# Kernel tuning notes

Measured on AMD Instinct MI355X. Metric: run time of the kernel, lower is better.

Reference implementation:

```python
import jax, jax.numpy as jnp
import numpy as np

N_NODES = 20000
N_EDGES = 320000
N_GRAPHS = 64
IN_FEAT = 64
HIDDEN = 256
GRID = 4
NUM_LAYERS = 4  # -> 3 Fourier message-passing layers
NEG_SLOPE = 0.01  # nn.LeakyReLU default


def setup_inputs() -> dict:
    key = jax.random.key(0)
    ks = jax.random.split(key, 8)
    h = jax.random.normal(ks[0], (N_NODES, IN_FEAT), dtype=jnp.float32)
    src = jax.random.randint(ks[1], (N_EDGES,), 0, N_NODES, dtype=jnp.int32)
    dst = jax.random.randint(ks[2], (N_EDGES,), 0, N_NODES, dtype=jnp.int32)
    graph_ids = jnp.sort(jax.random.randint(ks[3], (N_NODES,), 0, N_GRAPHS, dtype=jnp.int32))
    # KAN_polynomial(in_feat, hidden, degree=grid_feat), init randn/(sqrt(in)*sqrt(deg))
    W_line = jax.random.normal(ks[4], (HIDDEN, IN_FEAT, GRID + 1), dtype=jnp.float32) / (
        np.sqrt(IN_FEAT) * np.sqrt(GRID))
    # 3 NaiveFourierKANLayer coeffs [2, out, in, grid]
    fourier_coeffs = jax.random.normal(ks[5], (NUM_LAYERS - 1, 2, HIDDEN, HIDDEN, GRID),
                                       dtype=jnp.float32) / (np.sqrt(HIDDEN) * np.sqrt(GRID))
    # Readout KAN_polynomial(hidden, 1, degree=1, addbias=True)
    W_out = jax.random.normal(ks[6], (1, HIDDEN, 2), dtype=jnp.float32) / np.sqrt(HIDDEN)
    b_out = jnp.zeros((1, 1), dtype=jnp.float32)
    return {"h": h, "src": src, "dst": dst, "graph_ids": graph_ids,
            "W_line": W_line, "fourier_coeffs": fourier_coeffs,
            "W_out": W_out, "b_out": b_out}


def kan_polynomial(x, coeffs, bias=None):
    # x: [b, in], coeffs: [out, in, deg+1]
    deg = coeffs.shape[-1] - 1
    powers = jnp.stack([x ** i for i in range(deg + 1)], axis=-1)  # [b, in, deg+1]
    y = jnp.einsum('bid,oid->bo', powers, coeffs)
    if bias is not None:
        y = y + bias
    return y


def fourier_kan(x, coeffs):
    # x: [N, in], coeffs: [2, out, in, grid]
    grid = coeffs.shape[-1]
    k = jnp.arange(1, grid + 1, dtype=x.dtype)  # [grid]
    ang = x[:, :, None] * k  # [N, in, grid]
    y = jnp.einsum('nig,oig->no', jnp.cos(ang), coeffs[0])
    y = y + jnp.einsum('nig,oig->no', jnp.sin(ang), coeffs[1])
    return y


def reference(h, src, dst, graph_ids, W_line, fourier_coeffs, W_out, b_out):
    # kan_line
    h = kan_polynomial(h, W_line)  # [N, hidden]
    # message-passing Fourier KAN layers with residual + leaky_relu
    for l in range(NUM_LAYERS - 1):
        agg = jax.ops.segment_sum(h[src], dst, num_segments=N_NODES)  # copy_u + sum
        m = fourier_kan(agg, fourier_coeffs[l])
        h = jax.nn.leaky_relu(m + h, negative_slope=NEG_SLOPE)
    # avg pooling per graph
    sums = jax.ops.segment_sum(h, graph_ids, num_segments=N_GRAPHS)  # [G, hidden]
    counts = jax.ops.segment_sum(jnp.ones((N_NODES,), dtype=h.dtype), graph_ids,
                                 num_segments=N_GRAPHS)
    y = sums / jnp.maximum(counts, 1.0)[:, None]
    # Readout: KAN_polynomial(hidden, 1, degree=1) + sigmoid
    out = jax.nn.sigmoid(kan_polynomial(y, W_out, b_out))  # [G, 1]
    return out
```

## Files before the change

### kernel.cpp

```cpp
#include <hip/hip_runtime.h>
#include <math.h>

#define N_NODES   20000
#define N_PAD2    20096
#define N_EDGES   320000
#define N_GRAPHS  64
#define IN_FEAT   64
#define HIDDEN    256
#define GRID_F    4
#define NLAYERS   3
#define NEG_SLOPE 0.01f

#define KF 2048
#define KL4 256
#define NB_SCAN 79
#define NRG  157
#define NBLK (NRG * 4)
#define NLBLK 1256

typedef _Float16 f16x8 __attribute__((ext_vector_type(8)));
typedef _Float16 f16x2 __attribute__((ext_vector_type(2)));
typedef float    f32x4 __attribute__((ext_vector_type(4)));

__global__ void transpose_fourier_f16(const float* __restrict__ fc, _Float16* __restrict__ Bt) {
    int idx = blockIdx.x * 256 + threadIdx.x;
    int kk  = idx & 2047;
    int rest = idx >> 11;
    int o = rest & 255;
    int l = rest >> 8;
    int i = kk >> 3, f = kk & 7, g = f >> 1, t = f & 1;
    Bt[idx] = (_Float16)fc[(((size_t)(l * 2 + t) * HIDDEN + o) * HIDDEN + i) * GRID_F + g];
}

__global__ void transpose_line4(const float* __restrict__ wl, _Float16* __restrict__ Wth,
                                _Float16* __restrict__ Wtl) {
    int idx = blockIdx.x * 256 + threadIdx.x;
    int o = idx >> 8, kk = idx & 255;
    int i = kk >> 2, d = (kk & 3) + 1;
    float wv = wl[(o * IN_FEAT + i) * 5 + d];
    _Float16 h = (_Float16)wv;
    Wth[idx] = h;
    Wtl[idx] = (_Float16)(wv - (float)h);
}

__global__ void line_bias(const float* __restrict__ wl, float* __restrict__ biasv) {
    int o = threadIdx.x;
    float s = 0.f;
    for (int i = 0; i < IN_FEAT; ++i) s += wl[(o * IN_FEAT + i) * 5];
    biasv[o] = s;
}

__global__ void count_deg(const int* __restrict__ dst, int* __restrict__ counts) {
    int e = blockIdx.x * 256 + threadIdx.x;
    if (e < N_EDGES) atomicAdd(&counts[dst[e]], 1);
}

__global__ void block_sums(const int* __restrict__ counts, int* __restrict__ bsum) {
    int i = blockIdx.x * 256 + threadIdx.x;
    int v = (i < N_NODES) ? counts[i] : 0;
    #pragma unroll
    for (int o = 32; o > 0; o >>= 1) v += __shfl_down(v, o, 64);
    __shared__ int ws[4];
    if ((threadIdx.x & 63) == 0) ws[threadIdx.x >> 6] = v;
    __syncthreads();
    if (threadIdx.x == 0) bsum[blockIdx.x] = ws[0] + ws[1] + ws[2] + ws[3];
}

__global__ void scan_mid(const int* __restrict__ bsum, int* __restrict__ bofs,
                         int* __restrict__ row_start) {
    __shared__ int buf[128];
    int t = threadIdx.x;
    int v = (t < NB_SCAN) ? bsum[t] : 0;
    buf[t] = v;
    __syncthreads();
    for (int d = 1; d < 128; d <<= 1) {
        int x = (t >= d) ? buf[t - d] : 0;
        __syncthreads();
        buf[t] += x;
        __syncthreads();
    }
    if (t < NB_SCAN) bofs[t] = buf[t] - v;
    if (t == NB_SCAN - 1) row_start[N_NODES] = buf[t];
}

__global__ void scan_blocks(const int* __restrict__ counts, const int* __restrict__ bofs,
                            int* __restrict__ row_start) {
    int i = blockIdx.x * 256 + threadIdx.x;
    int val = (i < N_NODES) ? counts[i] : 0;
    int lane = threadIdx.x & 63, wid = threadIdx.x >> 6;
    int v = val;
    #pragma unroll
    for (int d = 1; d < 64; d <<= 1) {
        int t = __shfl_up(v, d, 64);
        if (lane >= d) v += t;
    }
    __shared__ int ws[4];
    if (lane == 63) ws[wid] = v;
    __syncthreads();
    int wofs = 0;
    for (int j = 0; j < wid; ++j) wofs += ws[j];
    if (i < N_NODES) row_start[i] = bofs[blockIdx.x] + wofs + v - val;
}

__global__ void fill_csr(const int* __restrict__ src, const int* __restrict__ dst,
                         const int* __restrict__ row_start, int* __restrict__ cursor,
                         int* __restrict__ ssrc) {
    int e = blockIdx.x * 256 + threadIdx.x;
    if (e < N_EDGES) {
        int d = dst[e];
        int pos = row_start[d] + atomicAdd(&cursor[d], 1);
        ssrc[pos] = src[e];
    }
}

__global__ __launch_bounds__(256)
void aggregate(const float* __restrict__ h, const int* __restrict__ row_start,
               const int* __restrict__ ssrc, float* __restrict__ agg) {
    const int node = blockIdx.x * 4 + (threadIdx.x >> 6);
    const int lane = threadIdx.x & 63;
    const int b = row_start[node], e = row_start[node + 1];
    f32x4 a0 = {0.f, 0.f, 0.f, 0.f}, a1 = {0.f, 0.f, 0.f, 0.f};
    int j = b;
    for (; j + 1 < e; j += 2) {
        int s0 = ssrc[j], s1 = ssrc[j + 1];
        a0 += *(const f32x4*)&h[(size_t)s0 * HIDDEN + lane * 4];
        a1 += *(const f32x4*)&h[(size_t)s1 * HIDDEN + lane * 4];
    }
    if (j < e) {
        int s0 = ssrc[j];
        a0 += *(const f32x4*)&h[(size_t)s0 * HIDDEN + lane * 4];
    }
    *(f32x4*)&agg[(size_t)node * HIDDEN + lane * 4] = a0 + a1;
}

__device__ __forceinline__ void makepow(float xa, float xb, f16x8& hi, f16x8& lo) {
    float p0 = xa, p1 = xa * xa;
    float p2 = p1 * xa, p3 = p1 * p1;
    float q0 = xb, q1 = xb * xb;
    float q2 = q1 * xb, q3 = q1 * q1;
    float pp[8] = {p0, p1, p2, p3, q0, q1, q2, q3};
    #pragma unroll
    for (int j = 0; j < 8; ++j) {
        _Float16 h = (_Float16)pp[j];
        hi[j] = h;
        lo[j] = (_Float16)(pp[j] - (float)h);
    }
}

__global__ __launch_bounds__(256)
void kan_line_mfma(const float* __restrict__ x, const _Float16* __restrict__ Wth,
                   const _Float16* __restrict__ Wtl, const float* __restrict__ biasv,
                   float* __restrict__ out) {
    __shared__ float    As[64][64];
    __shared__ _Float16 Bsh[64][136];
    __shared__ _Float16 Bsl[64][136];

    const int t = threadIdx.x;
    const int w = t >> 6, l = t & 63, ln = l & 15, quad = l >> 4;
    const int wr = w >> 1, wc = w & 1;

    const int g   = blockIdx.x;
    const int bid = (g & 7) * 157 + (g >> 3);
    const int Mbase = (bid >> 2) * 64;
    const int col0  = (bid & 3) * 64;

    #pragma unroll
    for (int r = 0; r < 4; ++r) {
        int idx = r * 256 + t;
        int row = idx >> 4, p = idx & 15;
        int grow = Mbase + row;
        if (grow > N_NODES - 1) grow = N_NODES - 1;
        f32x4 v = *(const f32x4*)&x[(size_t)grow * IN_FEAT + p * 4];
        *(f32x4*)&As[row][(p * 4) ^ ((row & 7) << 2)] = v;
    }
    const _Float16* WthB = Wth + (size_t)col0 * KL4;
    const _Float16* WtlB = Wtl + (size_t)col0 * KL4;
    #pragma unroll
    for (int r = 0; r < 4; ++r) {
        int idx = r * 256 + t;
        int c = idx >> 4, p = idx & 15;
        *(f16x8*)&Bsh[c][p * 8] = *(const f16x8*)&WthB[(size_t)c * KL4 + p * 8];
        *(f16x8*)&Bsl[c][p * 8] = *(const f16x8*)&WtlB[(size_t)c * KL4 + p * 8];
    }
    f16x8 pbh[4], pbl[4];
    #pragma unroll
    for (int r = 0; r < 4; ++r) {
        int idx = r * 256 + t;
        int c = idx >> 4, p = idx & 15;
        pbh[r] = *(const f16x8*)&WthB[(size_t)c * KL4 + 128 + p * 8];
        pbl[r] = *(const f16x8*)&WtlB[(size_t)c * KL4 + 128 + p * 8];
    }
    __syncthreads();

    f32x4 acc[2][2];
    #pragma unroll
    for (int rt = 0; rt < 2; ++rt)
        #pragma unroll
        for (int ct = 0; ct < 2; ++ct)
            acc[rt][ct] = (f32x4){0.f, 0.f, 0.f, 0.f};

    const int lr0 = wr * 32 + ln;
    const int xsw = (lr0 & 7) << 2;

    #pragma unroll
    for (int half = 0; half < 2; ++half) {
        #pragma unroll
        for (int kcl = 0; kcl < 4; ++kcl) {
            const int kc = half * 4 + kcl;
            const int f0 = kc * 8 + quad * 2;
            float x00 = As[lr0     ][f0 ^ xsw];
            float x01 = As[lr0     ][(f0 + 1) ^ xsw];
            float x10 = As[lr0 + 16][f0 ^ xsw];
            float x11 = As[lr0 + 16][(f0 + 1) ^ xsw];
            f16x8 ah0, al0, ah1, al1;
            makepow(x00, x01, ah0, al0);
            makepow(x10, x11, ah1, al1);
            #pragma unroll
            for (int ct = 0; ct < 2; ++ct) {
                const int bc = wc * 32 + ct * 16 + ln;
                f16x8 bh = *(const f16x8*)&Bsh[bc][kcl * 32 + quad * 8];
                f16x8 bl = *(const f16x8*)&Bsl[bc][kcl * 32 + quad * 8];
                acc[0][ct] = __builtin_amdgcn_mfma_f32_16x16x32_f16(ah0, bh, acc[0][ct], 0, 0, 0);
                acc[0][ct] = __builtin_amdgcn_mfma_f32_16x16x32_f16(al0, bh, acc[0][ct], 0, 0, 0);
                acc[0][ct] = __builtin_amdgcn_mfma_f32_16x16x32_f16(ah0, bl, acc[0][ct], 0, 0, 0);
                acc[1][ct] = __builtin_amdgcn_mfma_f32_16x16x32_f16(ah1, bh, acc[1][ct], 0, 0, 0);
                acc[1][ct] = __builtin_amdgcn_mfma_f32_16x16x32_f16(al1, bh, acc[1][ct], 0, 0, 0);
                acc[1][ct] = __builtin_amdgcn_mfma_f32_16x16x32_f16(ah1, bl, acc[1][ct], 0, 0, 0);
            }
        }
        if (half == 0) {
            __syncthreads();
            #pragma unroll
            for (int r = 0; r < 4; ++r) {
                int idx = r * 256 + t;
                int c = idx >> 4, p = idx & 15;
                *(f16x8*)&Bsh[c][p * 8] = pbh[r];
                *(f16x8*)&Bsl[c][p * 8] = pbl[r];
            }
            __syncthreads();
        }
    }

    #pragma unroll
    for (int rt = 0; rt < 2; ++rt) {
        const int row0 = Mbase + wr * 32 + rt * 16 + quad * 4;
        #pragma unroll
        for (int ct = 0; ct < 2; ++ct) {
            const int col = col0 + wc * 32 + ct * 16 + ln;
            const float bv = biasv[col];
            #pragma unroll
            for (int r = 0; r < 4; ++r) {
                const int row = row0 + r;
                if (row < N_NODES)
                    out[(size_t)row * HIDDEN + col] = acc[rt][ct][r] + bv;
            }
        }
    }
}

__device__ __forceinline__ f16x8 trig8i(float xv) {
    float r = xv * 0.15915494309189535f;
    r -= floorf(r);
    float s1 = __builtin_amdgcn_sinf(r);
    float c1 = __builtin_amdgcn_cosf(r);
    _Float16 c1h = (_Float16)c1, s1h = (_Float16)s1;
    f16x2 z1 = {c1h, s1h};
    f16x2 cc = {c1h, c1h};
    f16x2 ms = {(_Float16)-s1h, s1h};
    f16x2 z2 = z1 * cc + (f16x2){z1[1], z1[0]} * ms;
    f16x2 z3 = z2 * cc + (f16x2){z2[1], z2[0]} * ms;
    f16x2 z4 = z3 * cc + (f16x2){z3[1], z3[0]} * ms;
    union { f16x8 v; f16x2 p[4]; } u;
    u.p[0] = z1; u.p[1] = z2; u.p[2] = z3; u.p[3] = z4;
    return u.v;
}

__global__ __launch_bounds__(256)
void fourier_mfma(const float* __restrict__ agg, float* hio,
                  const _Float16* __restrict__ Bt) {
    __shared__ _Float16 Bs[2][64][140];
    __shared__ float    As[2][128][17];

    const int t    = threadIdx.x;
    const int w    = t >> 6;
    const int l    = t & 63;
    const int ln   = l & 15;
    const int quad = l >> 4;

    const int g   = blockIdx.x;
    const int xcd = g & 7, ii = g >> 3;
    const int bid = (xcd < 4 ? xcd * 79 : 316 + (xcd - 4) * 78) + ii;
    const int Mbase = (bid >> 2) * 128;
    const int col0  = (bid & 3) * 64;

    const int sc = t >> 4, sp = t & 15;
    const int sr = t >> 2, sq = t & 3;
    const _Float16* bg0 = Bt + (size_t)(col0 + sc) * KF + sp * 8;
    const _Float16* bg1 = bg0 + (size_t)16 * KF;
    const _Float16* bg2 = bg0 + (size_t)32 * KF;
    const _Float16* bg3 = bg0 + (size_t)48 * KF;
    const float* ag0 = agg + (size_t)(Mbase + sr) * HIDDEN + sq * 4;
    const float* ag1 = ag0 + (size_t)64 * HIDDEN;

    f32x4 acc[2][4];
    #pragma unroll
    for (int rt = 0; rt < 2; ++rt)
        #pragma unroll
        for (int ct = 0; ct < 4; ++ct)
            acc[rt][ct] = (f32x4){0.f, 0.f, 0.f, 0.f};

    f16x8 sb0, sb1, sb2, sb3;
    f32x4 sa0, sa1;

    sb0 = *(const f16x8*)(bg0);
    sb1 = *(const f16x8*)(bg1);
    sb2 = *(const f16x8*)(bg2);
    sb3 = *(const f16x8*)(bg3);
    sa0 = *(const f32x4*)(ag0);
    sa1 = *(const f32x4*)(ag1);
    *(f16x8*)&Bs[0][sc     ][sp * 8] = sb0;
    *(f16x8*)&Bs[0][sc + 16][sp * 8] = sb1;
    *(f16x8*)&Bs[0][sc + 32][sp * 8] = sb2;
    *(f16x8*)&Bs[0][sc + 48][sp * 8] = sb3;
    #pragma unroll
    for (int j = 0; j < 4; ++j) {
        As[0][sr     ][sq * 4 + j] = sa0[j];
        As[0][sr + 64][sq * 4 + j] = sa1[j];
    }
    __syncthreads();

    const int lr0 = w * 32 + ln;

    for (int kg = 0; kg < 16; ++kg) {
        const int b = kg & 1;
        if (kg < 15) {
            sb0 = *(const f16x8*)(bg0 + (kg + 1) * 128);
            sb1 = *(const f16x8*)(bg1 + (kg + 1) * 128);
            sb2 = *(const f16x8*)(bg2 + (kg + 1) * 128);
            sb3 = *(const f16x8*)(bg3 + (kg + 1) * 128);
            sa0 = *(const f32x4*)(ag0 + (kg + 1) * 16);
            sa1 = *(const f32x4*)(ag1 + (kg + 1) * 16);
        }
        #pragma unroll
        for (int kc = 0; kc < 4; ++kc) {
            float xv0 = As[b][lr0     ][kc * 4 + quad];
            float xv1 = As[b][lr0 + 16][kc * 4 + quad];
            f16x8 b0 = *(const f16x8*)&Bs[b][ln     ][kc * 32 + quad * 8];
            f16x8 b1 = *(const f16x8*)&Bs[b][ln + 16][kc * 32 + quad * 8];
            f16x8 b2 = *(const f16x8*)&Bs[b][ln + 32][kc * 32 + quad * 8];
            f16x8 b3 = *(const f16x8*)&Bs[b][ln + 48][kc * 32 + quad * 8];
            f16x8 a0 = trig8i(xv0);
            f16x8 a1 = trig8i(xv1);
            acc[0][0] = __builtin_amdgcn_mfma_f32_16x16x32_f16(a0, b0, acc[0][0], 0, 0, 0);
            acc[0][1] = __builtin_amdgcn_mfma_f32_16x16x32_f16(a0, b1, acc[0][1], 0, 0, 0);
            acc[0][2] = __builtin_amdgcn_mfma_f32_16x16x32_f16(a0, b2, acc[0][2], 0, 0, 0);
            acc[0][3] = __builtin_amdgcn_mfma_f32_16x16x32_f16(a0, b3, acc[0][3], 0, 0, 0);
            acc[1][0] = __builtin_amdgcn_mfma_f32_16x16x32_f16(a1, b0, acc[1][0], 0, 0, 0);
            acc[1][1] = __builtin_amdgcn_mfma_f32_16x16x32_f16(a1, b1, acc[1][1], 0, 0, 0);
            acc[1][2] = __builtin_amdgcn_mfma_f32_16x16x32_f16(a1, b2, acc[1][2], 0, 0, 0);
            acc[1][3] = __builtin_amdgcn_mfma_f32_16x16x32_f16(a1, b3, acc[1][3], 0, 0, 0);
        }
        __syncthreads();
        if (kg < 15) {
            const int nb = b ^ 1;
            *(f16x8*)&Bs[nb][sc     ][sp * 8] = sb0;
            *(f16x8*)&Bs[nb][sc + 16][sp * 8] = sb1;
            *(f16x8*)&Bs[nb][sc + 32][sp * 8] = sb2;
            *(f16x8*)&Bs[nb][sc + 48][sp * 8] = sb3;
            #pragma unroll
            for (int j = 0; j < 4; ++j) {
                As[nb][sr     ][sq * 4 + j] = sa0[j];
                As[nb][sr + 64][sq * 4 + j] = sa1[j];
            }
        }
        __syncthreads();
    }

    #pragma unroll
    for (int rt = 0; rt < 2; ++rt) {
        const int row0 = Mbase + w * 32 + rt * 16 + quad * 4;
        #pragma unroll
        for (int ct = 0; ct < 4; ++ct) {
            const int col = col0 + ct * 16 + ln;
            #pragma unroll
            for (int r = 0; r < 4; ++r) {
                const int row = row0 + r;
                if (row < N_NODES) {
                    float v = acc[rt][ct][r] + hio[(size_t)row * HIDDEN + col];
                    v = v > 0.f ? v : NEG_SLOPE * v;
                    hio[(size_t)row * HIDDEN + col] = v;
                }
            }
        }
    }
}

__global__ void graph_bounds(const int* __restrict__ gid, int* __restrict__ gstart) {
    int g = threadIdx.x;
    if (g < N_GRAPHS) {
        int lo = 0, hi = N_NODES;
        while (lo < hi) { int mid = (lo + hi) >> 1; if (gid[mid] < g) lo = mid + 1; else hi = mid; }
        gstart[g] = lo;
    } else if (g == N_GRAPHS) {
        gstart[g] = N_NODES;
    }
}

__global__ __launch_bounds__(256)
void pool_seg(const float* __restrict__ h, const int* __restrict__ gid,
              float* __restrict__ pooled) {
    const int c = threadIdx.x;
    const int s = blockIdx.x * 128;
    const int e = min(s + 128, N_NODES);
    float acc = 0.f;
    int g = gid[s];
    for (int n = s; n < e; ++n) {
        int gn = gid[n];
        if (gn != g) {
            atomicAdd(&pooled[g * HIDDEN + c], acc);
            acc = 0.f;
            g = gn;
        }
        acc += h[(size_t)n * HIDDEN + c];
    }
    atomicAdd(&pooled[g * HIDDEN + c], acc);
}

__global__ void readout(const float* __restrict__ pooled, const int* __restrict__ gstart,
                        const float* __restrict__ wout, const float* __restrict__ bout,
                        float* __restrict__ out) {
    int g = blockIdx.x, t = threadIdx.x;
    float cnt = fmaxf((float)(gstart[g + 1] - gstart[g]), 1.f);
    float y = pooled[g * HIDDEN + t] / cnt;
    float term = wout[t * 2 + 0] + wout[t * 2 + 1] * y;
    #pragma unroll
    for (int o = 32; o > 0; o >>= 1) term += __shfl_down(term, o, 64);
    __shared__ float wsum[4];
    if ((t & 63) == 0) wsum[t >> 6] = term;
    __syncthreads();
    if (t == 0) {
        float s = wsum[0] + wsum[1] + wsum[2] + wsum[3] + bout[0];
        out[g] = 1.f / (1.f + expf(-s));
    }
}

extern "C" void kernel_launch(void* const* d_in, const int* in_sizes, int n_in,
                              void* d_out, int out_size, void* d_ws, size_t ws_size,
                              hipStream_t stream) {
    const float* h_in  = (const float*)d_in[0];
    const int*   src   = (const int*)d_in[1];
    const int*   dst   = (const int*)d_in[2];
    const int*   gid   = (const int*)d_in[3];
    const float* wline = (const float*)d_in[4];
    const float* fcoef = (const float*)d_in[5];
    const float* wout  = (const float*)d_in[6];
    const float* bout  = (const float*)d_in[7];
    float* out = (float*)d_out;

    char* ws = (char*)d_ws;
    size_t off = 0;
    auto alloc = [&](size_t bytes) {
        size_t o = off;
        off += (bytes + 255) & ~size_t(255);
        return o;
    };
    float*     hbuf      = (float*)(ws + alloc((size_t)N_PAD2 * HIDDEN * 4));
    float*     aggbuf    = (float*)(ws + alloc((size_t)N_PAD2 * HIDDEN * 4));
    _Float16*  BtF16     = (_Float16*)(ws + alloc((size_t)NLAYERS * KF * HIDDEN * 2));
    _Float16*  Wth       = (_Float16*)(ws + alloc((size_t)HIDDEN * KL4 * 2));
    _Float16*  Wtl       = (_Float16*)(ws + alloc((size_t)HIDDEN * KL4 * 2));
    float*     biasv     = (float*)(ws + alloc((size_t)HIDDEN * 4));
    int*       row_start = (int*)(ws + alloc((size_t)(N_NODES + 1) * 4));
    int*       counts    = (int*)(ws + alloc((size_t)N_NODES * 4));
    int*       cursor    = (int*)(ws + alloc((size_t)N_NODES * 4));
    int*       ssrc      = (int*)(ws + alloc((size_t)N_EDGES * 4));
    int*       bsum      = (int*)(ws + alloc((size_t)128 * 4));
    int*       bofs      = (int*)(ws + alloc((size_t)128 * 4));
    int*       gstart    = (int*)(ws + alloc((size_t)(N_GRAPHS + 1) * 4));
    float*     pooled    = (float*)(ws + alloc((size_t)N_GRAPHS * HIDDEN * 4));

    hipMemsetAsync(counts, 0, (size_t)N_NODES * 4, stream);
    hipMemsetAsync(cursor, 0, (size_t)N_NODES * 4, stream);
    hipMemsetAsync(pooled, 0, (size_t)N_GRAPHS * HIDDEN * 4, stream);
    hipMemsetAsync(aggbuf + (size_t)N_NODES * HIDDEN, 0,
                   (size_t)(N_PAD2 - N_NODES) * HIDDEN * 4, stream);

    transpose_fourier_f16<<<6144, 256, 0, stream>>>(fcoef, BtF16);
    transpose_line4<<<256, 256, 0, stream>>>(wline, Wth, Wtl);
    line_bias<<<1, 256, 0, stream>>>(wline, biasv);
    count_deg<<<(N_EDGES + 255) / 256, 256, 0, stream>>>(dst, counts);
    block_sums<<<NB_SCAN, 256, 0, stream>>>(counts, bsum);
    scan_mid<<<1, 128, 0, stream>>>(bsum, bofs, row_start);
    scan_blocks<<<NB_SCAN, 256, 0, stream>>>(counts, bofs, row_start);
    fill_csr<<<(N_EDGES + 255) / 256, 256, 0, stream>>>(src, dst, row_start, cursor, ssrc);
    graph_bounds<<<1, 128, 0, stream>>>(gid, gstart);

    kan_line_mfma<<<NLBLK, 256, 0, stream>>>(h_in, Wth, Wtl, biasv, hbuf);

    for (int l = 0; l < NLAYERS; ++l) {
        aggregate<<<N_NODES / 4, 256, 0, stream>>>(hbuf, row_start, ssrc, aggbuf);
        fourier_mfma<<<NBLK, 256, 0, stream>>>(aggbuf, hbuf,
                                               BtF16 + (size_t)l * KF * HIDDEN);
    }

    pool_seg<<<(N_NODES + 127) / 128, 256, 0, stream>>>(hbuf, gid, pooled);
    readout<<<N_GRAPHS, 256, 0, stream>>>(pooled, gstart, wout, bout, out);
}
```

Before: 455.2 us.

## Precompute packed f16 cos/sin in aggregate epilogue and drop redundant barrier

The aggregate kernel now evaluates the base cos/sin of each aggregated value and stores them as a packed f16 pair. The Fourier GEMM then only expands the higher harmonics from that pair instead of recomputing the transcendentals. Before, each Fourier block recomputed the same trig values, repeated across the four column tiles. The GEMM loop also drops one of its two __syncthreads per k-step, which is safe because the buffer being refilled was last read before the previous barrier. The intermediate buffer stays the same size, so memory traffic is unchanged.

```diff
diff --git a/kernel.cpp b/kernel.cpp
--- a/kernel.cpp
+++ b/kernel.cpp
@@ -115,7 +115,7 @@
 
 __global__ __launch_bounds__(256)
 void aggregate(const float* __restrict__ h, const int* __restrict__ row_start,
-               const int* __restrict__ ssrc, float* __restrict__ agg) {
+               const int* __restrict__ ssrc, unsigned* __restrict__ cs) {
     const int node = blockIdx.x * 4 + (threadIdx.x >> 6);
     const int lane = threadIdx.x & 63;
     const int b = row_start[node], e = row_start[node + 1];
@@ -130,7 +130,19 @@
         int s0 = ssrc[j];
         a0 += *(const f32x4*)&h[(size_t)s0 * HIDDEN + lane * 4];
     }
-    *(f32x4*)&agg[(size_t)node * HIDDEN + lane * 4] = a0 + a1;
+    f32x4 v = a0 + a1;
+    unsigned csv[4];
+    #pragma unroll
+    for (int k = 0; k < 4; ++k) {
+        float r = v[k] * 0.15915494309189535f;
+        r -= floorf(r);
+        _Float16 ch = (_Float16)__builtin_amdgcn_cosf(r);
+        _Float16 sh = (_Float16)__builtin_amdgcn_sinf(r);
+        union { f16x2 z; unsigned u; } p;
+        p.z = (f16x2){ch, sh};
+        csv[k] = p.u;
+    }
+    *(uint4*)&cs[(size_t)node * HIDDEN + lane * 4] = make_uint4(csv[0], csv[1], csv[2], csv[3]);
 }
 
 __device__ __forceinline__ void makepow(float xa, float xb, f16x8& hi, f16x8& lo) {
@@ -258,15 +270,11 @@
     }
 }
 
-__device__ __forceinline__ f16x8 trig8i(float xv) {
-    float r = xv * 0.15915494309189535f;
-    r -= floorf(r);
-    float s1 = __builtin_amdgcn_sinf(r);
-    float c1 = __builtin_amdgcn_cosf(r);
-    _Float16 c1h = (_Float16)c1, s1h = (_Float16)s1;
-    f16x2 z1 = {c1h, s1h};
-    f16x2 cc = {c1h, c1h};
-    f16x2 ms = {(_Float16)-s1h, s1h};
+__device__ __forceinline__ f16x8 expand4(unsigned csu) {
+    union { unsigned u; f16x2 z; } w; w.u = csu;
+    f16x2 z1 = w.z;
+    f16x2 cc = {z1[0], z1[0]};
+    f16x2 ms = {(_Float16)(-z1[1]), z1[1]};
     f16x2 z2 = z1 * cc + (f16x2){z1[1], z1[0]} * ms;
     f16x2 z3 = z2 * cc + (f16x2){z2[1], z2[0]} * ms;
     f16x2 z4 = z3 * cc + (f16x2){z3[1], z3[0]} * ms;
@@ -276,10 +284,10 @@
 }
 
 __global__ __launch_bounds__(256)
-void fourier_mfma(const float* __restrict__ agg, float* hio,
+void fourier_mfma(const unsigned* __restrict__ cs, float* hio,
                   const _Float16* __restrict__ Bt) {
     __shared__ _Float16 Bs[2][64][140];
-    __shared__ float    As[2][128][17];
+    __shared__ unsigned As[2][128][17];
 
     const int t    = threadIdx.x;
     const int w    = t >> 6;
@@ -299,8 +307,8 @@
     const _Float16* bg1 = bg0 + (size_t)16 * KF;
     const _Float16* bg2 = bg0 + (size_t)32 * KF;
     const _Float16* bg3 = bg0 + (size_t)48 * KF;
-    const float* ag0 = agg + (size_t)(Mbase + sr) * HIDDEN + sq * 4;
-    const float* ag1 = ag0 + (size_t)64 * HIDDEN;
+    const unsigned* ag0 = cs + (size_t)(Mbase + sr) * HIDDEN + sq * 4;
+    const unsigned* ag1 = ag0 + (size_t)64 * HIDDEN;
 
     f32x4 acc[2][4];
     #pragma unroll
@@ -310,23 +318,26 @@
             acc[rt][ct] = (f32x4){0.f, 0.f, 0.f, 0.f};
 
     f16x8 sb0, sb1, sb2, sb3;
-    f32x4 sa0, sa1;
+    uint4 sa0, sa1;
 
     sb0 = *(const f16x8*)(bg0);
     sb1 = *(const f16x8*)(bg1);
     sb2 = *(const f16x8*)(bg2);
     sb3 = *(const f16x8*)(bg3);
-    sa0 = *(const f32x4*)(ag0);
-    sa1 = *(const f32x4*)(ag1);
+    sa0 = *(const uint4*)(ag0);
+    sa1 = *(const uint4*)(ag1);
     *(f16x8*)&Bs[0][sc     ][sp * 8] = sb0;
     *(f16x8*)&Bs[0][sc + 16][sp * 8] = sb1;
     *(f16x8*)&Bs[0][sc + 32][sp * 8] = sb2;
     *(f16x8*)&Bs[0][sc + 48][sp * 8] = sb3;
-    #pragma unroll
-    for (int j = 0; j < 4; ++j) {
-        As[0][sr     ][sq * 4 + j] = sa0[j];
-        As[0][sr + 64][sq * 4 + j] = sa1[j];
-    }
+    As[0][sr     ][sq * 4 + 0] = sa0.x;
+    As[0][sr     ][sq * 4 + 1] = sa0.y;
+    As[0][sr     ][sq * 4 + 2] = sa0.z;
+    As[0][sr     ][sq * 4 + 3] = sa0.w;
+    As[0][sr + 64][sq * 4 + 0] = sa1.x;
+    As[0][sr + 64][sq * 4 + 1] = sa1.y;
+    As[0][sr + 64][sq * 4 + 2] = sa1.z;
+    As[0][sr + 64][sq * 4 + 3] = sa1.w;
     __syncthreads();
 
     const int lr0 = w * 32 + ln;
@@ -338,19 +349,19 @@
             sb1 = *(const f16x8*)(bg1 + (kg + 1) * 128);
             sb2 = *(const f16x8*)(bg2 + (kg + 1) * 128);
             sb3 = *(const f16x8*)(bg3 + (kg + 1) * 128);
-            sa0 = *(const f32x4*)(ag0 + (kg + 1) * 16);
-            sa1 = *(const f32x4*)(ag1 + (kg + 1) * 16);
+            sa0 = *(const uint4*)(ag0 + (kg + 1) * 16);
+            sa1 = *(const uint4*)(ag1 + (kg + 1) * 16);
         }
         #pragma unroll
         for (int kc = 0; kc < 4; ++kc) {
-            float xv0 = As[b][lr0     ][kc * 4 + quad];
-            float xv1 = As[b][lr0 + 16][kc * 4 + quad];
+            unsigned cv0 = As[b][lr0     ][kc * 4 + quad];
+            unsigned cv1 = As[b][lr0 + 16][kc * 4 + quad];
             f16x8 b0 = *(const f16x8*)&Bs[b][ln     ][kc * 32 + quad * 8];
             f16x8 b1 = *(const f16x8*)&Bs[b][ln + 16][kc * 32 + quad * 8];
             f16x8 b2 = *(const f16x8*)&Bs[b][ln + 32][kc * 32 + quad * 8];
             f16x8 b3 = *(const f16x8*)&Bs[b][ln + 48][kc * 32 + quad * 8];
-            f16x8 a0 = trig8i(xv0);
-            f16x8 a1 = trig8i(xv1);
+            f16x8 a0 = expand4(cv0);
+            f16x8 a1 = expand4(cv1);
             acc[0][0] = __builtin_amdgcn_mfma_f32_16x16x32_f16(a0, b0, acc[0][0], 0, 0, 0);
             acc[0][1] = __builtin_amdgcn_mfma_f32_16x16x32_f16(a0, b1, acc[0][1], 0, 0, 0);
             acc[0][2] = __builtin_amdgcn_mfma_f32_16x16x32_f16(a0, b2, acc[0][2], 0, 0, 0);
@@ -360,18 +371,20 @@
             acc[1][2] = __builtin_amdgcn_mfma_f32_16x16x32_f16(a1, b2, acc[1][2], 0, 0, 0);
             acc[1][3] = __builtin_amdgcn_mfma_f32_16x16x32_f16(a1, b3, acc[1][3], 0, 0, 0);
         }
-        __syncthreads();
         if (kg < 15) {
             const int nb = b ^ 1;
             *(f16x8*)&Bs[nb][sc     ][sp * 8] = sb0;
             *(f16x8*)&Bs[nb][sc + 16][sp * 8] = sb1;
             *(f16x8*)&Bs[nb][sc + 32][sp * 8] = sb2;
             *(f16x8*)&Bs[nb][sc + 48][sp * 8] = sb3;
-            #pragma unroll
-            for (int j = 0; j < 4; ++j) {
-                As[nb][sr     ][sq * 4 + j] = sa0[j];
-                As[nb][sr + 64][sq * 4 + j] = sa1[j];
-            }
+            As[nb][sr     ][sq * 4 + 0] = sa0.x;
+            As[nb][sr     ][sq * 4 + 1] = sa0.y;
+            As[nb][sr     ][sq * 4 + 2] = sa0.z;
+            As[nb][sr     ][sq * 4 + 3] = sa0.w;
+            As[nb][sr + 64][sq * 4 + 0] = sa1.x;
+            As[nb][sr + 64][sq * 4 + 1] = sa1.y;
+            As[nb][sr + 64][sq * 4 + 2] = sa1.z;
+            As[nb][sr + 64][sq * 4 + 3] = sa1.w;
         }
         __syncthreads();
     }
@@ -465,7 +478,7 @@
         return o;
     };
     float*     hbuf      = (float*)(ws + alloc((size_t)N_PAD2 * HIDDEN * 4));
-    float*     aggbuf    = (float*)(ws + alloc((size_t)N_PAD2 * HIDDEN * 4));
+    unsigned*  csbuf     = (unsigned*)(ws + alloc((size_t)N_PAD2 * HIDDEN * 4));
     _Float16*  BtF16     = (_Float16*)(ws + alloc((size_t)NLAYERS * KF * HIDDEN * 2));
     _Float16*  Wth       = (_Float16*)(ws + alloc((size_t)HIDDEN * KL4 * 2));
     _Float16*  Wtl       = (_Float16*)(ws + alloc((size_t)HIDDEN * KL4 * 2));
@@ -482,7 +495,7 @@
     hipMemsetAsync(counts, 0, (size_t)N_NODES * 4, stream);
     hipMemsetAsync(cursor, 0, (size_t)N_NODES * 4, stream);
     hipMemsetAsync(pooled, 0, (size_t)N_GRAPHS * HIDDEN * 4, stream);
-    hipMemsetAsync(aggbuf + (size_t)N_NODES * HIDDEN, 0,
+    hipMemsetAsync(csbuf + (size_t)N_NODES * HIDDEN, 0,
                    (size_t)(N_PAD2 - N_NODES) * HIDDEN * 4, stream);
 
     transpose_fourier_f16<<<6144, 256, 0, stream>>>(fcoef, BtF16);
@@ -498,8 +511,8 @@
     kan_line_mfma<<<NLBLK, 256, 0, stream>>>(h_in, Wth, Wtl, biasv, hbuf);
 
     for (int l = 0; l < NLAYERS; ++l) {
-        aggregate<<<N_NODES / 4, 256, 0, stream>>>(hbuf, row_start, ssrc, aggbuf);
-        fourier_mfma<<<NBLK, 256, 0, stream>>>(aggbuf, hbuf,
+        aggregate<<<N_NODES / 4, 256, 0, stream>>>(hbuf, row_start, ssrc, csbuf);
+        fourier_mfma<<<NBLK, 256, 0, stream>>>(csbuf, hbuf,
                                                BtF16 + (size_t)l * KF * HIDDEN);
     }
 
```

Measured after the change: 441.3 us. -3.1%, faster.
